# Performance work log

Hardware: AMD Instinct MI355X
Metric: run time of the kernel (lower is better)

The kernel has to match this reference:

```python
import jax, jax.numpy as jnp
import numpy as np

N_NODES = 100000
N_EDGES = 1000000
D = 128          # node_dim == out_dim (embedding_dim)
EDGE_DIM = 10
NEG_SLOPE = 0.01  # torch leaky_relu default
EPS = 1e-16       # PyG softmax denominator eps


def _leaky(x):
    return jnp.where(x >= 0, x, NEG_SLOPE * x)


def setup_inputs() -> dict:
    key = jax.random.key(0)
    ks = jax.random.split(key, 12)
    s = lambda fan_in: 1.0 / np.sqrt(fan_in)
    return {
        "x": jax.random.normal(ks[0], (N_NODES, D), jnp.float32),
        "edge_index": jax.random.randint(ks[1], (2, N_EDGES), 0, N_NODES),
        "edge_attr": jax.random.normal(ks[2], (N_EDGES, EDGE_DIM), jnp.float32),
        # q: Linear(D, D, bias=False)
        "Wq": jax.random.uniform(ks[3], (D, D), jnp.float32, -s(D), s(D)),
        # k: Linear(EDGE_DIM, D, bias=False)
        "Wk": jax.random.uniform(ks[4], (D, EDGE_DIM), jnp.float32, -s(EDGE_DIM), s(EDGE_DIM)),
        # v: Linear(EDGE_DIM, D) with bias
        "Wv": jax.random.uniform(ks[5], (D, EDGE_DIM), jnp.float32, -s(EDGE_DIM), s(EDGE_DIM)),
        "bv": jax.random.uniform(ks[6], (D,), jnp.float32, -s(EDGE_DIM), s(EDGE_DIM)),
        # attn_score_layer: Linear(2D, D) -> ReLU -> Linear(D, 1)
        "W1": jax.random.uniform(ks[7], (D, 2 * D), jnp.float32, -s(2 * D), s(2 * D)),
        "b1": jax.random.uniform(ks[8], (D,), jnp.float32, -s(2 * D), s(2 * D)),
        "W2": jax.random.uniform(ks[9], (1, D), jnp.float32, -s(D), s(D)),
        "b2": jax.random.uniform(ks[10], (1,), jnp.float32, -s(D), s(D)),
    }


def reference(x, edge_index, edge_attr, Wq, Wk, Wv, bv, W1, b1, W2, b2):
    N = x.shape[0]
    tgt = edge_index[1]                       # destination node per edge [E]
    q = x @ Wq.T                              # [N, D] node queries
    x_i = q[tgt]                              # gather target queries [E, D]
    k = _leaky(edge_attr @ Wk.T)              # [E, D]
    v = _leaky(edge_attr @ Wv.T + bv)         # [E, D]
    h = jnp.concatenate([x_i, k], axis=-1)    # [E, 2D]
    scores = (jax.nn.relu(h @ W1.T + b1) @ W2.T + b2)[:, 0]  # [E]
    # segment softmax over edges grouped by target node (PyG softmax)
    smax = jax.ops.segment_max(scores, tgt, num_segments=N)  # [N]
    e = jnp.exp(scores - smax[tgt])
    denom = jax.ops.segment_sum(e, tgt, num_segments=N)
    attn = e / (denom[tgt] + EPS)             # [E]
    out = jax.ops.segment_sum(v * attn[:, None], tgt, num_segments=N)  # [N, D]
    return out, attn
```

## Files before the change

### kernel.cpp

```cpp
#include <hip/hip_runtime.h>
#include <stdint.h>

#define NN 100000
#define NE 1000000
#define NTILES (NE / 64)
#define NB_SCAN 391

typedef __attribute__((ext_vector_type(8))) short bf16x8;
typedef __attribute__((ext_vector_type(4))) float f32x4;

static const size_t OFF_W1K   = 0;
static const size_t OFF_WVK   = 8192;
static const size_t OFF_W1BP  = 16384;
static const size_t OFF_MTB   = 49152;
static const size_t OFF_RP    = 81920;
static const size_t OFF_CUR   = 524288;
static const size_t OFF_PART  = 1048576;
static const size_t OFF_BSUM  = 1572864;
static const size_t OFF_BSUMX = 1576960;
static const size_t OFF_CNT   = 1581056;
static const size_t OFF_PT    = 2097152;
static const size_t OFF_EVALS = 10485760;
static const size_t OFF_EAS   = 14485760;
static const size_t OFF_SNODE = 34485760;

__device__ inline unsigned short f2bf(float f) {
    const unsigned int u = __float_as_uint(f);
    return (unsigned short)((u + 0x7fffu + ((u >> 16) & 1u)) >> 16);
}

__device__ inline unsigned int cvtpk(float lo, float hi) {
    unsigned int r;
    asm("v_cvt_pk_bf16_f32 %0, %1, %2" : "=v"(r) : "v"(lo), "v"(hi));
    return r;
}

__device__ inline float lk2(float v) {
    return fmaf(0.495f, fabsf(v), 0.505f * v);
}

union BU { bf16x8 v; uint4 u; };

__global__ __launch_bounds__(128) void prep_kernel(
    const float* __restrict__ W1, const float* __restrict__ Wq,
    const float* __restrict__ Wk, const float* __restrict__ Wv,
    unsigned short* __restrict__ w1k, unsigned short* __restrict__ wvk,
    unsigned short* __restrict__ w1bp, unsigned short* __restrict__ mtb,
    int* __restrict__ cnt)
{
    const int l = blockIdx.x;
    const int i = threadIdx.x;
    for (int z = l * 128 + i; z < NN; z += 128 * 128) cnt[z] = 0;
    float acc = 0.f;
#pragma unroll 8
    for (int j = 0; j < 128; ++j)
        acc = fmaf(W1[i * 256 + j], Wq[j * 128 + l], acc);
    mtb[i * 128 + l] = f2bf(acc);
    if (i < 32) {
        w1k[l * 32 + i] = (i < 10) ? f2bf(Wk[l * 10 + i]) : (unsigned short)0;
        wvk[l * 32 + i] = (i < 10) ? f2bf(Wv[l * 10 + i]) : (unsigned short)0;
    }
    const int m = l;
    const int j = (m & ~31) + 16 * ((m >> 2) & 1) + 4 * ((m >> 3) & 3) + (m & 3);
    w1bp[i * 128 + m] = f2bf(W1[i * 256 + 128 + j]);
}

__global__ __launch_bounds__(256) void node_score_kernel(
    const float* __restrict__ x, const unsigned short* __restrict__ mtb_g,
    const float* __restrict__ b1, unsigned short* __restrict__ s_node)
{
    __shared__ __align__(16) unsigned short mt_s[128 * 136];
    const int t = threadIdx.x;
    for (int idx = t; idx < 2048; idx += 256) {
        const uint4 v = ((const uint4*)mtb_g)[idx];
        const int row = idx >> 4, q = idx & 15;
        *(uint4*)&mt_s[row * 136 + q * 8] = v;
    }
    __syncthreads();

    const int lane = t & 63;
    const int wave = t >> 6;
    const int h    = lane >> 4;
    const int e15  = lane & 15;
    const int node = blockIdx.x * 64 + wave * 16 + e15;
    const int nc   = min(node, NN - 1);
    const int lds_base = e15 * 136 + h * 8;

    const f32x4 z4 = {0.f, 0.f, 0.f, 0.f};
    f32x4 acc[8];
#pragma unroll
    for (int g = 0; g < 8; ++g) acc[g] = z4;

#pragma unroll
    for (int s = 0; s < 4; ++s) {
        const float4 xa = *(const float4*)&x[(size_t)nc * 128 + s * 32 + h * 8];
        const float4 xb = *(const float4*)&x[(size_t)nc * 128 + s * 32 + h * 8 + 4];
        BU bx;
        bx.u.x = cvtpk(xa.x, xa.y);
        bx.u.y = cvtpk(xa.z, xa.w);
        bx.u.z = cvtpk(xb.x, xb.y);
        bx.u.w = cvtpk(xb.z, xb.w);
#pragma unroll
        for (int g = 0; g < 8; ++g) {
            const bf16x8 a = *(const bf16x8*)&mt_s[lds_base + g * (16 * 136) + s * 32];
            acc[g] = __builtin_amdgcn_mfma_f32_16x16x32_bf16(a, bx.v, acc[g], 0, 0, 0);
        }
    }

    if (node < NN) {
#pragma unroll
        for (int g = 0; g < 8; ++g) {
            const float4 bb = *(const float4*)&b1[g * 16 + h * 4];
            uint2 o2;
            o2.x = cvtpk(acc[g][0] + bb.x, acc[g][1] + bb.y);
            o2.y = cvtpk(acc[g][2] + bb.z, acc[g][3] + bb.w);
            *(uint2*)&s_node[(size_t)node * 128 + g * 16 + h * 4] = o2;
        }
    }
}

__global__ __launch_bounds__(256) void hist_kernel(
    const int* __restrict__ tgt, int* __restrict__ cnt)
{
    const int e = blockIdx.x * 256 + threadIdx.x;
    if (e < NE) atomicAdd(&cnt[tgt[e]], 1);
}

__global__ __launch_bounds__(256) void scan1_kernel(
    const int* __restrict__ cnt, int* __restrict__ part, int* __restrict__ bsum)
{
    __shared__ int s[256];
    const int t = threadIdx.x;
    const int idx = blockIdx.x * 256 + t;
    const int v = (idx < NN) ? cnt[idx] : 0;
    s[t] = v;
    __syncthreads();
    for (int off = 1; off < 256; off <<= 1) {
        const int u = (t >= off) ? s[t - off] : 0;
        __syncthreads();
        s[t] += u;
        __syncthreads();
    }
    part[idx] = s[t] - v;
    if (t == 255) bsum[blockIdx.x] = s[255];
}

__global__ __launch_bounds__(512) void scan2_kernel(
    const int* __restrict__ bsum, int* __restrict__ bsumx)
{
    __shared__ int s[512];
    const int t = threadIdx.x;
    const int v = (t < NB_SCAN) ? bsum[t] : 0;
    s[t] = v;
    __syncthreads();
    for (int off = 1; off < 512; off <<= 1) {
        const int u = (t >= off) ? s[t - off] : 0;
        __syncthreads();
        s[t] += u;
        __syncthreads();
    }
    if (t < NB_SCAN) bsumx[t] = s[t] - v;
}

__global__ __launch_bounds__(256) void scan3_kernel(
    const int* __restrict__ part, const int* __restrict__ bsumx,
    int* __restrict__ rowptr, int* __restrict__ cursor)
{
    const int idx = blockIdx.x * 256 + threadIdx.x;
    if (idx < NN) {
        const int rp = part[idx] + bsumx[idx >> 8];
        rowptr[idx] = rp;
        cursor[idx] = rp;
    }
    if (idx == 0) rowptr[NN] = NE;
}

__global__ __launch_bounds__(256) void fill_kernel(
    const int* __restrict__ tgt, int* __restrict__ cursor, int2* __restrict__ pt)
{
    const int e = blockIdx.x * 256 + threadIdx.x;
    if (e < NE) {
        const int tg = tgt[e];
        const int p  = atomicAdd(&cursor[tg], 1);
        pt[p] = make_int2(e, tg);
    }
}

__global__ __launch_bounds__(256) void edge_kernel(
    const float* __restrict__ edge_attr, const int2* __restrict__ pt,
    const unsigned short* __restrict__ w1k_g, const unsigned short* __restrict__ w1bp_g,
    const float* __restrict__ W2, const float* __restrict__ b2,
    const unsigned short* __restrict__ s_node,
    float* __restrict__ e_vals, unsigned int* __restrict__ eas)
{
    __shared__ __align__(16) unsigned short w1b_s[128 * 136];

    const int t = threadIdx.x;
    for (int idx = t; idx < 2048; idx += 256) {
        const uint4 v = ((const uint4*)w1bp_g)[idx];
        const int row = idx >> 4, q = idx & 15;
        *(uint4*)&w1b_s[row * 136 + q * 8] = v;
    }

    const int lane = t & 63;
    const int wave = t >> 6;
    const int h    = lane >> 4;
    const int e15  = lane & 15;

    bf16x8 a1[8];
#pragma unroll
    for (int f = 0; f < 8; ++f)
        a1[f] = *(const bf16x8*)&w1k_g[(f * 16 + e15) * 32 + h * 8];
    const float b2v = b2[0];

    __syncthreads();

    const int lds_base = e15 * 136 + h * 8;
    const int cstep    = gridDim.x * 64;

    int c = blockIdx.x * 64 + wave * 16 + e15;

    int2 ptc = pt[min(c, NE - 1)];
    int2 ptn = pt[min(c + cstep, NE - 1)];

    uint2 sn[8];
#pragma unroll
    for (int g = 0; g < 8; ++g)
        sn[g] = *(const uint2*)&s_node[(size_t)ptc.y * 128 + g * 16 + h * 4];

    float ea0 = 0.f, ea1 = 0.f, ea2 = 0.f, ea3 = 0.f, ea4 = 0.f;
    float ea5 = 0.f, ea6 = 0.f, ea7 = 0.f, ea8 = 0.f, ea9 = 0.f;
    {
        const float* pa = edge_attr + (size_t)ptc.x * 10;
        if (h == 0) {
            const float2 u0 = *(const float2*)(pa + 0);
            const float2 u1 = *(const float2*)(pa + 2);
            const float2 u2 = *(const float2*)(pa + 4);
            const float2 u3 = *(const float2*)(pa + 6);
            ea0 = u0.x; ea1 = u0.y; ea2 = u1.x; ea3 = u1.y;
            ea4 = u2.x; ea5 = u2.y; ea6 = u3.x; ea7 = u3.y;
        } else if (h == 1) {
            const float2 u4 = *(const float2*)(pa + 8);
            ea8 = u4.x; ea9 = u4.y;
        }
    }

    for (int tile = blockIdx.x; tile < NTILES; tile += gridDim.x, c += cstep) {
        const int2 ptn2 = pt[min(c + 2 * cstep, NE - 1)];
        uint2 sn_n[8];
#pragma unroll
        for (int g = 0; g < 8; ++g)
            sn_n[g] = *(const uint2*)&s_node[(size_t)ptn.y * 128 + g * 16 + h * 4];
        float en0 = 0.f, en1 = 0.f, en2 = 0.f, en3 = 0.f, en4 = 0.f;
        float en5 = 0.f, en6 = 0.f, en7 = 0.f, en8 = 0.f, en9 = 0.f;
        {
            const float* pa = edge_attr + (size_t)ptn.x * 10;
            if (h == 0) {
                const float2 u0 = *(const float2*)(pa + 0);
                const float2 u1 = *(const float2*)(pa + 2);
                const float2 u2 = *(const float2*)(pa + 4);
                const float2 u3 = *(const float2*)(pa + 6);
                en0 = u0.x; en1 = u0.y; en2 = u1.x; en3 = u1.y;
                en4 = u2.x; en5 = u2.y; en6 = u3.x; en7 = u3.y;
            } else if (h == 1) {
                const float2 u4 = *(const float2*)(pa + 8);
                en8 = u4.x; en9 = u4.y;
            }
        }

        bf16x8 b1 = (bf16x8){0, 0, 0, 0, 0, 0, 0, 0};
        {
            unsigned int* po = eas + (size_t)c * 5;
            if (h == 0) {
                BU bu;
                bu.u.x = cvtpk(ea0, ea1);
                bu.u.y = cvtpk(ea2, ea3);
                bu.u.z = cvtpk(ea4, ea5);
                bu.u.w = cvtpk(ea6, ea7);
                b1 = bu.v;
                po[0] = bu.u.x; po[1] = bu.u.y; po[2] = bu.u.z; po[3] = bu.u.w;
            } else if (h == 1) {
                BU bu;
                bu.u.x = cvtpk(ea8, ea9);
                bu.u.y = 0; bu.u.z = 0; bu.u.w = 0;
                b1 = bu.v;
                po[4] = bu.u.x;
            }
        }

        const f32x4 z4 = {0.f, 0.f, 0.f, 0.f};
        f32x4 acc1[8];
#pragma unroll
        for (int f = 0; f < 8; ++f)
            acc1[f] = __builtin_amdgcn_mfma_f32_16x16x32_bf16(a1[f], b1, z4, 0, 0, 0);

        bf16x8 pb[4];
#pragma unroll
        for (int s = 0; s < 4; ++s) {
            BU bu;
            bu.u.x = cvtpk(lk2(acc1[2 * s][0]), lk2(acc1[2 * s][1]));
            bu.u.y = cvtpk(lk2(acc1[2 * s][2]), lk2(acc1[2 * s][3]));
            bu.u.z = cvtpk(lk2(acc1[2 * s + 1][0]), lk2(acc1[2 * s + 1][1]));
            bu.u.w = cvtpk(lk2(acc1[2 * s + 1][2]), lk2(acc1[2 * s + 1][3]));
            pb[s] = bu.v;
        }

        float p = 0.f;
#pragma unroll
        for (int g2 = 0; g2 < 4; ++g2) {
            const int gA = 2 * g2, gB = 2 * g2 + 1;
            const uint2 svA = sn[gA], svB = sn[gB];
            f32x4 accA, accB;
            accA[0] = __uint_as_float(svA.x << 16);
            accA[1] = __uint_as_float(svA.x & 0xffff0000u);
            accA[2] = __uint_as_float(svA.y << 16);
            accA[3] = __uint_as_float(svA.y & 0xffff0000u);
            accB[0] = __uint_as_float(svB.x << 16);
            accB[1] = __uint_as_float(svB.x & 0xffff0000u);
            accB[2] = __uint_as_float(svB.y << 16);
            accB[3] = __uint_as_float(svB.y & 0xffff0000u);
#pragma unroll
            for (int s = 0; s < 4; ++s) {
                const bf16x8 a2A = *(const bf16x8*)&w1b_s[lds_base + gA * (16 * 136) + s * 32];
                const bf16x8 a2B = *(const bf16x8*)&w1b_s[lds_base + gB * (16 * 136) + s * 32];
                accA = __builtin_amdgcn_mfma_f32_16x16x32_bf16(a2A, pb[s], accA, 0, 0, 0);
                accB = __builtin_amdgcn_mfma_f32_16x16x32_bf16(a2B, pb[s], accB, 0, 0, 0);
            }
            const float4 w2A = *(const float4*)&W2[gA * 16 + h * 4];
            const float4 w2B = *(const float4*)&W2[gB * 16 + h * 4];
            p = fmaf(fmaxf(accA[0], 0.f), w2A.x, p);
            p = fmaf(fmaxf(accA[1], 0.f), w2A.y, p);
            p = fmaf(fmaxf(accA[2], 0.f), w2A.z, p);
            p = fmaf(fmaxf(accA[3], 0.f), w2A.w, p);
            p = fmaf(fmaxf(accB[0], 0.f), w2B.x, p);
            p = fmaf(fmaxf(accB[1], 0.f), w2B.y, p);
            p = fmaf(fmaxf(accB[2], 0.f), w2B.z, p);
            p = fmaf(fmaxf(accB[3], 0.f), w2B.w, p);
        }
        p += __shfl_xor(p, 16);
        p += __shfl_xor(p, 32);
        if (lane < 16)
            e_vals[c - e15 + lane] = __expf(p + b2v);

        ptc = ptn; ptn = ptn2;
#pragma unroll
        for (int g = 0; g < 8; ++g) sn[g] = sn_n[g];
        ea0 = en0; ea1 = en1; ea2 = en2; ea3 = en3; ea4 = en4;
        ea5 = en5; ea6 = en6; ea7 = en7; ea8 = en8; ea9 = en9;
    }
}

__global__ __launch_bounds__(256) void denom_kernel(
    const int* __restrict__ rowptr, const float* __restrict__ e_vals,
    float* __restrict__ inv_denom, float* __restrict__ out)
{
    const int n = blockIdx.x * 256 + threadIdx.x;
    if (n >= NN) return;
    const int rs = rowptr[n], re = rowptr[n + 1];
    float s = 0.f;
    for (int c = rs; c < re; ++c) s += e_vals[c];
    inv_denom[n] = 1.f / (s + 1e-16f);
    if (re > rs && (rs >> 6) != ((re - 1) >> 6)) {
        const float4 z = make_float4(0.f, 0.f, 0.f, 0.f);
        float4* po = (float4*)&out[(size_t)n * 128];
#pragma unroll 8
        for (int q = 0; q < 32; ++q) po[q] = z;
    }
}

__global__ __launch_bounds__(256) void vscatter_kernel(
    const int* __restrict__ rowptr, const int2* __restrict__ pt,
    const unsigned int* __restrict__ eas, const float* __restrict__ e_vals,
    const float* __restrict__ inv_denom,
    const unsigned short* __restrict__ wvk_g, const float* __restrict__ bv,
    float* __restrict__ out, float* __restrict__ attn_out)
{
    __shared__ __align__(16) float w_lds[64 * 132];

    const int t    = threadIdx.x;
    const int lane = t & 63;
    const int wv   = t >> 6;
    const int h    = lane >> 4;
    const int e15  = lane & 15;
    const int el   = wv * 16 + e15;

    bf16x8 av[8];
    float4 bb[8];
#pragma unroll
    for (int g = 0; g < 8; ++g) {
        av[g] = *(const bf16x8*)&wvk_g[(g * 16 + e15) * 32 + h * 8];
        bb[g] = *(const float4*)&bv[g * 16 + h * 4];
    }

    for (int tile = blockIdx.x; tile < NTILES; tile += gridDim.x) {
        const int base = tile * 64;
        const int c    = base + el;

        const int2 pc = pt[c];
        const float at = e_vals[c] * inv_denom[pc.y];
        if (h == 0) attn_out[pc.x] = at;

        bf16x8 be = (bf16x8){0, 0, 0, 0, 0, 0, 0, 0};
        {
            const unsigned int* pe = eas + (size_t)c * 5;
            if (h == 0) {
                BU bu;
                bu.u.x = pe[0]; bu.u.y = pe[1]; bu.u.z = pe[2]; bu.u.w = pe[3];
                be = bu.v;
            } else if (h == 1) {
                BU bu;
                bu.u.x = pe[4]; bu.u.y = 0; bu.u.z = 0; bu.u.w = 0;
                be = bu.v;
            }
        }

        __syncthreads();
#pragma unroll
        for (int g = 0; g < 8; ++g) {
            f32x4 cb;
            cb[0] = bb[g].x; cb[1] = bb[g].y; cb[2] = bb[g].z; cb[3] = bb[g].w;
            const f32x4 acc = __builtin_amdgcn_mfma_f32_16x16x32_bf16(av[g], be, cb, 0, 0, 0);
            float4 w;
            w.x = at * lk2(acc[0]);
            w.y = at * lk2(acc[1]);
            w.z = at * lk2(acc[2]);
            w.w = at * lk2(acc[3]);
            *(float4*)&w_lds[el * 132 + g * 16 + h * 4] = w;
        }
        __syncthreads();

        const int n_lo = (tile == 0) ? 0 : pt[base].y;
        const int n_hi = (tile == NTILES - 1) ? (NN - 1) : pt[base + 64].y;

        for (int nd = n_lo + wv; nd <= n_hi; nd += 4) {
            const int rs = rowptr[nd], re = rowptr[nd + 1];
            const int lo = max(rs, base), hi = min(re, base + 64);
            float sx = 0.f, sy = 0.f;
            for (int cc = lo; cc < hi; ++cc) {
                const float2 v = *(const float2*)&w_lds[(cc - base) * 132 + lane * 2];
                sx += v.x; sy += v.y;
            }
            float* po = &out[(size_t)nd * 128 + lane * 2];
            if (rs >= base && re <= base + 64) {
                *(float2*)po = make_float2(sx, sy);
            } else {
                atomicAdd(po, sx);
                atomicAdd(po + 1, sy);
            }
        }
    }
}

extern "C" void kernel_launch(void* const* d_in, const int* in_sizes, int n_in,
                              void* d_out, int out_size, void* d_ws, size_t ws_size,
                              hipStream_t stream)
{
    const float* x         = (const float*)d_in[0];
    const int*   eidx      = (const int*)d_in[1];
    const float* edge_attr = (const float*)d_in[2];
    const float* Wq        = (const float*)d_in[3];
    const float* Wk        = (const float*)d_in[4];
    const float* Wv        = (const float*)d_in[5];
    const float* bv        = (const float*)d_in[6];
    const float* W1        = (const float*)d_in[7];
    const float* b1        = (const float*)d_in[8];
    const float* W2        = (const float*)d_in[9];
    const float* b2        = (const float*)d_in[10];
    const int*   tgt       = eidx + NE;

    char* ws = (char*)d_ws;
    unsigned short* w1k    = (unsigned short*)(ws + OFF_W1K);
    unsigned short* wvk    = (unsigned short*)(ws + OFF_WVK);
    unsigned short* w1bp   = (unsigned short*)(ws + OFF_W1BP);
    unsigned short* mtb    = (unsigned short*)(ws + OFF_MTB);
    int*            rowptr = (int*)(ws + OFF_RP);
    int*            cursor = (int*)(ws + OFF_CUR);
    float*          invd   = (float*)(ws + OFF_CUR);
    int*            part   = (int*)(ws + OFF_PART);
    int*            bsum   = (int*)(ws + OFF_BSUM);
    int*            bsumx  = (int*)(ws + OFF_BSUMX);
    int*            cnt    = (int*)(ws + OFF_CNT);
    int2*           pt     = (int2*)(ws + OFF_PT);
    float*          e_vals = (float*)(ws + OFF_EVALS);
    unsigned int*   eas    = (unsigned int*)(ws + OFF_EAS);
    unsigned short* s_node = (unsigned short*)(ws + OFF_SNODE);

    float* out      = (float*)d_out;
    float* attn_out = out + (size_t)NN * 128;

    prep_kernel<<<128, 128, 0, stream>>>(W1, Wq, Wk, Wv, w1k, wvk, w1bp, mtb, cnt);
    node_score_kernel<<<(NN + 63) / 64, 256, 0, stream>>>(x, mtb, b1, s_node);
    hist_kernel<<<(NE + 255) / 256, 256, 0, stream>>>(tgt, cnt);
    scan1_kernel<<<NB_SCAN, 256, 0, stream>>>(cnt, part, bsum);
    scan2_kernel<<<1, 512, 0, stream>>>(bsum, bsumx);
    scan3_kernel<<<NB_SCAN, 256, 0, stream>>>(part, bsumx, rowptr, cursor);
    fill_kernel<<<(NE + 255) / 256, 256, 0, stream>>>(tgt, cursor, pt);
    edge_kernel<<<768, 256, 0, stream>>>(edge_attr, pt, w1k, w1bp, W2, b2,
                                         s_node, e_vals, eas);
    denom_kernel<<<(NN + 255) / 256, 256, 0, stream>>>(rowptr, e_vals, invd, out);
    vscatter_kernel<<<1024, 256, 0, stream>>>(rowptr, pt, eas, e_vals, invd,
                                              wvk, bv, out, attn_out);
}
```

Baseline: 297.0 us.

## Switch edge score MFMAs to 32x32x16 tiles and fuse histogram into prep

Reworks the edge scoring kernel to process 128 edges per block with 32x32x16 bf16 MFMAs instead of 16x16x32, re-permuting the W1 edge-half weights and the Wk packing to match the new operand layout. Larger MFMA tiles should mean fewer instructions and fewer LDS weight reads per edge, at the cost of more registers per lane (16 prefetched s_node chunks). The edge histogram is moved into extra blocks of the prep kernel and the count buffer is cleared with a memset, which removes one kernel launch.

```diff
diff --git a/kernel.cpp b/kernel.cpp
--- a/kernel.cpp
+++ b/kernel.cpp
@@ -3,11 +3,13 @@
 
 #define NN 100000
 #define NE 1000000
+#define NT2 7813
 #define NTILES (NE / 64)
 #define NB_SCAN 391
 
 typedef __attribute__((ext_vector_type(8))) short bf16x8;
 typedef __attribute__((ext_vector_type(4))) float f32x4;
+typedef __attribute__((ext_vector_type(16))) float f32x16;
 
 static const size_t OFF_W1K   = 0;
 static const size_t OFF_WVK   = 8192;
@@ -46,23 +48,30 @@
     const float* __restrict__ Wk, const float* __restrict__ Wv,
     unsigned short* __restrict__ w1k, unsigned short* __restrict__ wvk,
     unsigned short* __restrict__ w1bp, unsigned short* __restrict__ mtb,
-    int* __restrict__ cnt)
-{
+    const int* __restrict__ tgt, int* __restrict__ cnt)
+{
+    if (blockIdx.x >= 128) {
+        for (int e = (blockIdx.x - 128) * 128 + threadIdx.x; e < NE; e += 384 * 128)
+            atomicAdd(&cnt[tgt[e]], 1);
+        return;
+    }
     const int l = blockIdx.x;
     const int i = threadIdx.x;
-    for (int z = l * 128 + i; z < NN; z += 128 * 128) cnt[z] = 0;
     float acc = 0.f;
 #pragma unroll 8
     for (int j = 0; j < 128; ++j)
         acc = fmaf(W1[i * 256 + j], Wq[j * 128 + l], acc);
     mtb[i * 128 + l] = f2bf(acc);
-    if (i < 32) {
-        w1k[l * 32 + i] = (i < 10) ? f2bf(Wk[l * 10 + i]) : (unsigned short)0;
+    if (i < 16)
+        w1k[l * 16 + i] = (i < 10) ? f2bf(Wk[l * 10 + i]) : (unsigned short)0;
+    if (i < 32)
         wvk[l * 32 + i] = (i < 10) ? f2bf(Wv[l * 10 + i]) : (unsigned short)0;
-    }
     const int m = l;
-    const int j = (m & ~31) + 16 * ((m >> 2) & 1) + 4 * ((m >> 3) & 3) + (m & 3);
-    w1bp[i * 128 + m] = f2bf(W1[i * 256 + 128 + j]);
+    const int s  = m >> 4;
+    const int h5 = (m >> 3) & 1;
+    const int jj = m & 7;
+    const int jn = 32 * (s >> 1) + 8 * ((s & 1) + 2 * (jj >> 2)) + (jj & 3) + 4 * h5;
+    w1bp[i * 128 + m] = f2bf(W1[i * 256 + 128 + jn]);
 }
 
 __global__ __launch_bounds__(256) void node_score_kernel(
@@ -119,13 +128,6 @@
     }
 }
 
-__global__ __launch_bounds__(256) void hist_kernel(
-    const int* __restrict__ tgt, int* __restrict__ cnt)
-{
-    const int e = blockIdx.x * 256 + threadIdx.x;
-    if (e < NE) atomicAdd(&cnt[tgt[e]], 1);
-}
-
 __global__ __launch_bounds__(256) void scan1_kernel(
     const int* __restrict__ cnt, int* __restrict__ part, int* __restrict__ bsum)
 {
@@ -204,65 +206,63 @@
 
     const int lane = t & 63;
     const int wave = t >> 6;
-    const int h    = lane >> 4;
-    const int e15  = lane & 15;
-
-    bf16x8 a1[8];
-#pragma unroll
-    for (int f = 0; f < 8; ++f)
-        a1[f] = *(const bf16x8*)&w1k_g[(f * 16 + e15) * 32 + h * 8];
+    const int h5   = lane >> 5;
+    const int e31  = lane & 31;
+
+    bf16x8 a1[4];
+#pragma unroll
+    for (int f = 0; f < 4; ++f)
+        a1[f] = *(const bf16x8*)&w1k_g[(f * 32 + e31) * 16 + h5 * 8];
     const float b2v = b2[0];
 
     __syncthreads();
 
-    const int lds_base = e15 * 136 + h * 8;
-    const int cstep    = gridDim.x * 64;
-
-    int c = blockIdx.x * 64 + wave * 16 + e15;
+    const int cstep = gridDim.x * 128;
+    int c = blockIdx.x * 128 + wave * 32 + e31;
 
     int2 ptc = pt[min(c, NE - 1)];
     int2 ptn = pt[min(c + cstep, NE - 1)];
 
-    uint2 sn[8];
-#pragma unroll
-    for (int g = 0; g < 8; ++g)
-        sn[g] = *(const uint2*)&s_node[(size_t)ptc.y * 128 + g * 16 + h * 4];
+    uint2 sn[16];
+#pragma unroll
+    for (int q = 0; q < 16; ++q)
+        sn[q] = *(const uint2*)&s_node[(size_t)ptc.y * 128 + (q >> 2) * 32 + (q & 3) * 8 + h5 * 4];
 
     float ea0 = 0.f, ea1 = 0.f, ea2 = 0.f, ea3 = 0.f, ea4 = 0.f;
     float ea5 = 0.f, ea6 = 0.f, ea7 = 0.f, ea8 = 0.f, ea9 = 0.f;
     {
         const float* pa = edge_attr + (size_t)ptc.x * 10;
-        if (h == 0) {
+        if (h5 == 0) {
             const float2 u0 = *(const float2*)(pa + 0);
             const float2 u1 = *(const float2*)(pa + 2);
             const float2 u2 = *(const float2*)(pa + 4);
             const float2 u3 = *(const float2*)(pa + 6);
             ea0 = u0.x; ea1 = u0.y; ea2 = u1.x; ea3 = u1.y;
             ea4 = u2.x; ea5 = u2.y; ea6 = u3.x; ea7 = u3.y;
-        } else if (h == 1) {
+        } else {
             const float2 u4 = *(const float2*)(pa + 8);
             ea8 = u4.x; ea9 = u4.y;
         }
     }
 
-    for (int tile = blockIdx.x; tile < NTILES; tile += gridDim.x, c += cstep) {
+    for (int tile = blockIdx.x; tile < NT2; tile += gridDim.x, c += cstep) {
         const int2 ptn2 = pt[min(c + 2 * cstep, NE - 1)];
-        uint2 sn_n[8];
-#pragma unroll
-        for (int g = 0; g < 8; ++g)
-            sn_n[g] = *(const uint2*)&s_node[(size_t)ptn.y * 128 + g * 16 + h * 4];
+        uint2 sn_n[16];
+#pragma unroll
+        for (int q = 0; q < 16; ++q)
+            sn_n[q] = *(const uint2*)&s_node[(size_t)ptn.y * 128 + (q >> 2) * 32 + (q & 3) * 8 + h5 * 4];
         float en0 = 0.f, en1 = 0.f, en2 = 0.f, en3 = 0.f, en4 = 0.f;
         float en5 = 0.f, en6 = 0.f, en7 = 0.f, en8 = 0.f, en9 = 0.f;
         {
             const float* pa = edge_attr + (size_t)ptn.x * 10;
-            if (h == 0) {
+            if (h5 == 0) {
                 const float2 u0 = *(const float2*)(pa + 0);
                 const float2 u1 = *(const float2*)(pa + 2);
                 const float2 u2 = *(const float2*)(pa + 4);
                 const float2 u3 = *(const float2*)(pa + 6);
                 en0 = u0.x; en1 = u0.y; en2 = u1.x; en3 = u1.y;
                 en4 = u2.x; en5 = u2.y; en6 = u3.x; en7 = u3.y;
-            } else if (h == 1) {
+            } else {
                 const float2 u4 = *(const float2*)(pa + 8);
                 en8 = u4.x; en9 = u4.y;
             }
@@ -271,80 +271,74 @@
         bf16x8 b1 = (bf16x8){0, 0, 0, 0, 0, 0, 0, 0};
         {
             unsigned int* po = eas + (size_t)c * 5;
-            if (h == 0) {
+            if (h5 == 0) {
                 BU bu;
                 bu.u.x = cvtpk(ea0, ea1);
                 bu.u.y = cvtpk(ea2, ea3);
                 bu.u.z = cvtpk(ea4, ea5);
                 bu.u.w = cvtpk(ea6, ea7);
                 b1 = bu.v;
-                po[0] = bu.u.x; po[1] = bu.u.y; po[2] = bu.u.z; po[3] = bu.u.w;
-            } else if (h == 1) {
+                if (c < NE) { po[0] = bu.u.x; po[1] = bu.u.y; po[2] = bu.u.z; po[3] = bu.u.w; }
+            } else {
                 BU bu;
                 bu.u.x = cvtpk(ea8, ea9);
                 bu.u.y = 0; bu.u.z = 0; bu.u.w = 0;
                 b1 = bu.v;
-                po[4] = bu.u.x;
-            }
-        }
-
-        const f32x4 z4 = {0.f, 0.f, 0.f, 0.f};
-        f32x4 acc1[8];
-#pragma unroll
-        for (int f = 0; f < 8; ++f)
-            acc1[f] = __builtin_amdgcn_mfma_f32_16x16x32_bf16(a1[f], b1, z4, 0, 0, 0);
-
-        bf16x8 pb[4];
-#pragma unroll
-        for (int s = 0; s < 4; ++s) {
-            BU bu;
-            bu.u.x = cvtpk(lk2(acc1[2 * s][0]), lk2(acc1[2 * s][1]));
-            bu.u.y = cvtpk(lk2(acc1[2 * s][2]), lk2(acc1[2 * s][3]));
-            bu.u.z = cvtpk(lk2(acc1[2 * s + 1][0]), lk2(acc1[2 * s + 1][1]));
-            bu.u.w = cvtpk(lk2(acc1[2 * s + 1][2]), lk2(acc1[2 * s + 1][3]));
-            pb[s] = bu.v;
+                if (c < NE) po[4] = bu.u.x;
+            }
+        }
+
+        f32x16 z16;
+#pragma unroll
+        for (int q = 0; q < 16; ++q) z16[q] = 0.f;
+        bf16x8 pb[8];
+#pragma unroll
+        for (int f = 0; f < 4; ++f) {
+            const f32x16 a1r = __builtin_amdgcn_mfma_f32_32x32x16_bf16(a1[f], b1, z16, 0, 0, 0);
+#pragma unroll
+            for (int rho = 0; rho < 2; ++rho) {
+                BU bu;
+                bu.u.x = cvtpk(lk2(a1r[4 * rho + 0]), lk2(a1r[4 * rho + 1]));
+                bu.u.y = cvtpk(lk2(a1r[4 * rho + 2]), lk2(a1r[4 * rho + 3]));
+                bu.u.z = cvtpk(lk2(a1r[4 * rho + 8]), lk2(a1r[4 * rho + 9]));
+                bu.u.w = cvtpk(lk2(a1r[4 * rho + 10]), lk2(a1r[4 * rho + 11]));
+                pb[2 * f + rho] = bu.v;
+            }
         }
 
         float p = 0.f;
 #pragma unroll
-        for (int g2 = 0; g2 < 4; ++g2) {
-            const int gA = 2 * g2, gB = 2 * g2 + 1;
-            const uint2 svA = sn[gA], svB = sn[gB];
-            f32x4 accA, accB;
-            accA[0] = __uint_as_float(svA.x << 16);
-            accA[1] = __uint_as_float(svA.x & 0xffff0000u);
-            accA[2] = __uint_as_float(svA.y << 16);
-            accA[3] = __uint_as_float(svA.y & 0xffff0000u);
-            accB[0] = __uint_as_float(svB.x << 16);
-            accB[1] = __uint_as_float(svB.x & 0xffff0000u);
-            accB[2] = __uint_as_float(svB.y << 16);
-            accB[3] = __uint_as_float(svB.y & 0xffff0000u);
-#pragma unroll
-            for (int s = 0; s < 4; ++s) {
-                const bf16x8 a2A = *(const bf16x8*)&w1b_s[lds_base + gA * (16 * 136) + s * 32];
-                const bf16x8 a2B = *(const bf16x8*)&w1b_s[lds_base + gB * (16 * 136) + s * 32];
-                accA = __builtin_amdgcn_mfma_f32_16x16x32_bf16(a2A, pb[s], accA, 0, 0, 0);
-                accB = __builtin_amdgcn_mfma_f32_16x16x32_bf16(a2B, pb[s], accB, 0, 0, 0);
-            }
-            const float4 w2A = *(const float4*)&W2[gA * 16 + h * 4];
-            const float4 w2B = *(const float4*)&W2[gB * 16 + h * 4];
-            p = fmaf(fmaxf(accA[0], 0.f), w2A.x, p);
-            p = fmaf(fmaxf(accA[1], 0.f), w2A.y, p);
-            p = fmaf(fmaxf(accA[2], 0.f), w2A.z, p);
-            p = fmaf(fmaxf(accA[3], 0.f), w2A.w, p);
-            p = fmaf(fmaxf(accB[0], 0.f), w2B.x, p);
-            p = fmaf(fmaxf(accB[1], 0.f), w2B.y, p);
-            p = fmaf(fmaxf(accB[2], 0.f), w2B.z, p);
-            p = fmaf(fmaxf(accB[3], 0.f), w2B.w, p);
-        }
-        p += __shfl_xor(p, 16);
+        for (int g = 0; g < 4; ++g) {
+            f32x16 acc2;
+#pragma unroll
+            for (int u = 0; u < 4; ++u) {
+                const uint2 sv = sn[g * 4 + u];
+                acc2[4 * u + 0] = __uint_as_float(sv.x << 16);
+                acc2[4 * u + 1] = __uint_as_float(sv.x & 0xffff0000u);
+                acc2[4 * u + 2] = __uint_as_float(sv.y << 16);
+                acc2[4 * u + 3] = __uint_as_float(sv.y & 0xffff0000u);
+            }
+#pragma unroll
+            for (int s = 0; s < 8; ++s) {
+                const bf16x8 a2 = *(const bf16x8*)&w1b_s[(g * 32 + e31) * 136 + s * 16 + h5 * 8];
+                acc2 = __builtin_amdgcn_mfma_f32_32x32x16_bf16(a2, pb[s], acc2, 0, 0, 0);
+            }
+#pragma unroll
+            for (int u = 0; u < 4; ++u) {
+                const float4 w2v = *(const float4*)&W2[g * 32 + u * 8 + h5 * 4];
+                p = fmaf(fmaxf(acc2[4 * u + 0], 0.f), w2v.x, p);
+                p = fmaf(fmaxf(acc2[4 * u + 1], 0.f), w2v.y, p);
+                p = fmaf(fmaxf(acc2[4 * u + 2], 0.f), w2v.z, p);
+                p = fmaf(fmaxf(acc2[4 * u + 3], 0.f), w2v.w, p);
+            }
+        }
         p += __shfl_xor(p, 32);
-        if (lane < 16)
-            e_vals[c - e15 + lane] = __expf(p + b2v);
+        if (lane < 32 && c < NE)
+            e_vals[c] = __expf(p + b2v);
 
         ptc = ptn; ptn = ptn2;
 #pragma unroll
-        for (int g = 0; g < 8; ++g) sn[g] = sn_n[g];
+        for (int q = 0; q < 16; ++q) sn[q] = sn_n[q];
         ea0 = en0; ea1 = en1; ea2 = en2; ea3 = en3; ea4 = en4;
         ea5 = en5; ea6 = en6; ea7 = en7; ea8 = en8; ea9 = en9;
     }
@@ -488,9 +482,11 @@
     float* out      = (float*)d_out;
     float* attn_out = out + (size_t)NN * 128;
 
-    prep_kernel<<<128, 128, 0, stream>>>(W1, Wq, Wk, Wv, w1k, wvk, w1bp, mtb, cnt);
+    hipMemsetAsync(cnt, 0, (size_t)NN * sizeof(int), stream);
+
+    prep_kernel<<<512, 128, 0, stream>>>(W1, Wq, Wk, Wv, w1k, wvk, w1bp, mtb,
+                                         tgt, cnt);
     node_score_kernel<<<(NN + 63) / 64, 256, 0, stream>>>(x, mtb, b1, s_node);
-    hist_kernel<<<(NE + 255) / 256, 256, 0, stream>>>(tgt, cnt);
     scan1_kernel<<<NB_SCAN, 256, 0, stream>>>(cnt, part, bsum);
     scan2_kernel<<<1, 512, 0, stream>>>(bsum, bsumx);
     scan3_kernel<<<NB_SCAN, 256, 0, stream>>>(part, bsumx, rowptr, cursor);
```

New measurement: 293.2 us. Within noise of the previous version (-1.3%).
